# Kernel optimization log

Hardware: AMD Instinct MI355X
Metric: run time of the kernel (lower is better)

The kernel has to match this reference:

```python
import jax, jax.numpy as jnp
import numpy as np

N = 65536   # nodes
E = 524288  # edges (avg degree 8)
IN, H, Z = 256, 128, 32
LN_EPS = 1e-5


def setup_inputs() -> dict:
    key = jax.random.key(0)
    ks = jax.random.split(key, 6)
    x = jax.random.normal(ks[0], (N, IN), jnp.float32)
    edge_index = jax.random.randint(ks[1], (2, E), 0, N, jnp.int32)
    W1 = jax.random.normal(ks[2], (IN, H), jnp.float32) / np.sqrt(IN)
    W2 = jax.random.normal(ks[3], (H, H), jnp.float32) / np.sqrt(H)
    W3 = jax.random.normal(ks[4], (H, Z), jnp.float32) / np.sqrt(H)
    return dict(
        x=x, edge_index=edge_index,
        ln_w=jnp.ones((IN,), jnp.float32), ln_b=jnp.zeros((IN,), jnp.float32),
        W1=W1, b1=jnp.zeros((H,), jnp.float32),
        W2=W2, b2=jnp.zeros((H,), jnp.float32),
        W3=W3, b3=jnp.zeros((Z,), jnp.float32),
    )


def _layer_norm(x, w, b):
    mu = jnp.mean(x, axis=-1, keepdims=True)
    var = jnp.mean(jnp.square(x - mu), axis=-1, keepdims=True)
    return (x - mu) * jax.lax.rsqrt(var + LN_EPS) * w + b


def _gcn_conv(x, W, b, src, dst, n):
    # PyG GCNConv: transform, add self-loops, symmetric deg normalization, scatter-add.
    x = x @ W  # [N, out]
    ones = jnp.ones(src.shape[0], x.dtype)
    deg = jax.ops.segment_sum(ones, dst, num_segments=n) + 1.0  # +1 self-loop
    dis = jax.lax.rsqrt(deg)  # deg^{-1/2}
    norm = dis[src] * dis[dst]  # [E]
    agg = jax.ops.segment_sum(x[src] * norm[:, None], dst, num_segments=n)
    agg = agg + x * (dis * dis)[:, None]  # self-loop term: dis[i]*dis[i]
    return agg + b


def reference(x, edge_index, ln_w, ln_b, W1, b1, W2, b2, W3, b3):
    src, dst = edge_index[0], edge_index[1]
    n = x.shape[0]
    h = _layer_norm(x, ln_w, ln_b)
    h = jax.nn.relu(_gcn_conv(h, W1, b1, src, dst, n))
    # dropout is identity in eval mode
    h = jax.nn.relu(_gcn_conv(h, W2, b2, src, dst, n))
    return _gcn_conv(h, W3, b3, src, dst, n)
```

## Files before the change

### kernel.cpp

```cpp
#include <hip/hip_runtime.h>
#include <hip/hip_bf16.h>

#define FIN 256
#define FH 128
#define FZ 32

typedef unsigned short u16;
typedef unsigned int u32;
typedef __attribute__((ext_vector_type(4))) float f32x4;
typedef __attribute__((ext_vector_type(8))) _Float16 f16x8;
typedef __attribute__((ext_vector_type(4))) _Float16 f16x4;
typedef __attribute__((ext_vector_type(4))) unsigned int uint4v;

__device__ inline u16 f2h(float v) { return __builtin_bit_cast(u16, (_Float16)v); }

__global__ __launch_bounds__(256) void prep(const float* __restrict__ W1,
                                            const float* __restrict__ W2,
                                            const float* __restrict__ W3,
                                            u16* __restrict__ w1h, u16* __restrict__ w2h,
                                            u16* __restrict__ w3h, int* __restrict__ deg,
                                            int* __restrict__ total) {
    int b = blockIdx.x, t = threadIdx.x;
    if (b < 256) {
        deg[b * 256 + t] = 0;
        if (b == 0 && t == 0) *total = 0;
        return;
    }
    int i = (b - 256) * 256 + t;
    if (i < FIN * FH) {
        int k = i / FH, n = i % FH;
        w1h[n * FIN + k] = f2h(W1[i]);
    } else if (i < FIN * FH + FH * FH) {
        int j = i - FIN * FH;
        int k = j / FH, n = j % FH;
        w2h[n * FH + k] = f2h(W2[j]);
    } else {
        int j = i - (FIN * FH + FH * FH);
        int k = j / FZ, n = j % FZ;
        w3h[n * FH + k] = f2h(W3[j]);
    }
}

__global__ void deg_count(const int* __restrict__ dst, int* __restrict__ deg,
                          int* __restrict__ erank, int E) {
    int e = blockIdx.x * 256 + threadIdx.x;
    if (e < E) erank[e] = atomicAdd(&deg[dst[e]], 1);
}

__global__ __launch_bounds__(256) void scan_fused(const int* __restrict__ deg,
                                                  int* __restrict__ total,
                                                  int* __restrict__ rowstart,
                                                  float* __restrict__ dis) {
    __shared__ int s[256];
    __shared__ int base;
    int t = threadIdx.x;
    int i = blockIdx.x * 256 + t;
    int v = deg[i];
    s[t] = v;
    __syncthreads();
    for (int o = 1; o < 256; o <<= 1) {
        int add = (t >= o) ? s[t - o] : 0;
        __syncthreads();
        s[t] += add;
        __syncthreads();
    }
    if (t == 255) base = atomicAdd(total, s[255]);
    __syncthreads();
    rowstart[i] = s[t] - v + base;
    dis[i] = rsqrtf((float)v + 1.0f);
}

template <int K, int N, bool LN, bool FILL>
__global__ __launch_bounds__(512) void gemm_v5(
    const float* __restrict__ Xf, const u16* __restrict__ Xh, const u16* __restrict__ Wg,
    const float* __restrict__ lnw, const float* __restrict__ lnb,
    const float* __restrict__ dis, u16* __restrict__ Y,
    const int* __restrict__ src, const int* __restrict__ dst,
    const int* __restrict__ erank, const int* __restrict__ rowstart,
    int* __restrict__ csrc, int E) {
    constexpr int BM = 128;
    constexpr int NT = N / 16;

    extern __shared__ char smem[];
    u16* Wl = (u16*)smem;
    float* stats = (float*)(smem + (size_t)N * K * 2);
    float* lnwl = stats + (LN ? BM * 2 : 0);
    float* lnbl = lnwl + (LN ? K : 0);

    const int t = threadIdx.x;
    const int row0 = blockIdx.x * BM;

    if (FILL) {
        int epb = E / gridDim.x;
        int base = blockIdx.x * epb;
#pragma unroll
        for (int j = 0; j < 2; ++j) {
            int e = base + j * 512 + t;
            int d = dst[e];
            csrc[rowstart[d] + erank[e]] = src[e];
        }
    }

    for (int i = t; i < N * K / 8; i += 512) {
        int n = i / (K / 8), k8 = i % (K / 8);
        *(uint4v*)&Wl[n * K + ((k8 ^ (n & 7)) * 8)] = *(const uint4v*)&Wg[n * K + k8 * 8];
    }

    if (LN) {
        if (t < K / 4) {
            *(f32x4*)&lnwl[t * 4] = *(const f32x4*)&lnw[t * 4];
            *(f32x4*)&lnbl[t * 4] = *(const f32x4*)&lnb[t * 4];
        }
        int r = t >> 2, q = t & 3;
        const float* xr = Xf + (long long)(row0 + r) * K + q * (K / 4);
        float s = 0.f, ss = 0.f;
#pragma unroll
        for (int j = 0; j < K / 16; ++j) {
            f32x4 f = *(const f32x4*)(xr + j * 4);
#pragma unroll
            for (int c = 0; c < 4; ++c) {
                s += f[c];
                ss += f[c] * f[c];
            }
        }
        s += __shfl_xor(s, 1);
        ss += __shfl_xor(ss, 1);
        s += __shfl_xor(s, 2);
        ss += __shfl_xor(ss, 2);
        if (q == 0) {
            float mu = s * (1.0f / K);
            float var = ss * (1.0f / K) - mu * mu;
            stats[r * 2] = mu;
            stats[r * 2 + 1] = rsqrtf(fmaxf(var, 0.f) + 1e-5f);
        }
    }
    __syncthreads();

    const int wave = t >> 6, l = t & 63;
    const int lm = l & 15, lq = l >> 4;
    const int row = row0 + wave * 16 + lm;

    float mu = 0.f, rs = 1.f;
    if (LN) {
        mu = stats[(wave * 16 + lm) * 2];
        rs = stats[(wave * 16 + lm) * 2 + 1];
    }

    f32x4 acc[NT];
#pragma unroll
    for (int i = 0; i < NT; ++i) acc[i] = (f32x4){0.f, 0.f, 0.f, 0.f};

#pragma unroll
    for (int kk = 0; kk < K / 32; ++kk) {
        f16x8 a;
        if (LN) {
            const float* xr = Xf + (long long)row * K;
            f32x4 a0 = *(const f32x4*)(xr + kk * 32 + lq * 8);
            f32x4 a1 = *(const f32x4*)(xr + kk * 32 + lq * 8 + 4);
            f32x4 w0 = *(const f32x4*)&lnwl[kk * 32 + lq * 8];
            f32x4 w1 = *(const f32x4*)&lnwl[kk * 32 + lq * 8 + 4];
            f32x4 c0 = *(const f32x4*)&lnbl[kk * 32 + lq * 8];
            f32x4 c1 = *(const f32x4*)&lnbl[kk * 32 + lq * 8 + 4];
#pragma unroll
            for (int c = 0; c < 4; ++c) {
                a[c] = (_Float16)((a0[c] - mu) * rs * w0[c] + c0[c]);
                a[4 + c] = (_Float16)((a1[c] - mu) * rs * w1[c] + c1[c]);
            }
        } else {
            a = *(const f16x8*)&Xh[(long long)row * K + kk * 32 + lq * 8];
        }

#pragma unroll
        for (int nt = 0; nt < NT; ++nt) {
            int n = nt * 16 + lm;
            int off = n * K + (((kk * 4 + lq) ^ (n & 7)) * 8);
            f16x8 bh = *(const f16x8*)&Wl[off];
            acc[nt] = __builtin_amdgcn_mfma_f32_16x16x32_f16(a, bh, acc[nt], 0, 0, 0);
        }
    }

    const int mbase = row0 + wave * 16 + lq * 4;
    f32x4 d4 = *(const f32x4*)(dis + mbase);
#pragma unroll
    for (int nt = 0; nt < NT; ++nt) {
        int c = nt * 16 + lm;
#pragma unroll
        for (int r = 0; r < 4; ++r) Y[(long long)(mbase + r) * N + c] = f2h(acc[nt][r] * d4[r]);
    }
}

__global__ __launch_bounds__(256) void agg128h(
    const u16* __restrict__ T, const int* __restrict__ rowstart, const int* __restrict__ degv,
    const int* __restrict__ csrc, const float* __restrict__ dis, const float* __restrict__ bias,
    u16* __restrict__ OUT, int relu) {
    int node = blockIdx.x * 4 + (threadIdx.x >> 6);
    int l = threadIdx.x & 63;
    int h = l >> 4, c = l & 15;
    float di = dis[node];
    float acc[8] = {0.f, 0.f, 0.f, 0.f, 0.f, 0.f, 0.f, 0.f};
    if (h == 0) {
        f16x8 s = *(const f16x8*)&T[(long long)node * 128 + c * 8];
#pragma unroll
        for (int i = 0; i < 8; ++i) acc[i] = (float)s[i];
    }
    int e0 = rowstart[node];
    int e1 = e0 + degv[node];
    int e = e0 + h;
    for (; e + 4 < e1; e += 8) {
        int s0 = csrc[e], s1 = csrc[e + 4];
        f16x8 u0 = *(const f16x8*)&T[(long long)s0 * 128 + c * 8];
        f16x8 u1 = *(const f16x8*)&T[(long long)s1 * 128 + c * 8];
#pragma unroll
        for (int i = 0; i < 8; ++i) acc[i] += (float)u0[i] + (float)u1[i];
    }
    if (e < e1) {
        int s0 = csrc[e];
        f16x8 u0 = *(const f16x8*)&T[(long long)s0 * 128 + c * 8];
#pragma unroll
        for (int i = 0; i < 8; ++i) acc[i] += (float)u0[i];
    }
#pragma unroll
    for (int m = 16; m <= 32; m <<= 1) {
#pragma unroll
        for (int i = 0; i < 8; ++i) acc[i] += __shfl_xor(acc[i], m);
    }
    if (h == 0) {
        f32x4 b0 = *(const f32x4*)(bias + c * 8);
        f32x4 b1 = *(const f32x4*)(bias + c * 8 + 4);
        f16x8 r;
#pragma unroll
        for (int i = 0; i < 8; ++i) {
            float b = (i < 4) ? b0[i] : b1[i - 4];
            float v = acc[i] * di + b;
            if (relu) v = fmaxf(v, 0.f);
            r[i] = (_Float16)v;
        }
        *(f16x8*)&OUT[(long long)node * 128 + c * 8] = r;
    }
}

__global__ __launch_bounds__(256) void agg32h(
    const u16* __restrict__ T, const int* __restrict__ rowstart, const int* __restrict__ degv,
    const int* __restrict__ csrc, const float* __restrict__ dis, const float* __restrict__ bias,
    float* __restrict__ OUT) {
    int node = blockIdx.x * 4 + (threadIdx.x >> 6);
    int l = threadIdx.x & 63;
    int h = l >> 3, c = l & 7;
    float di = dis[node];
    f32x4 acc = (f32x4){0.f, 0.f, 0.f, 0.f};
    if (h == 0) {
        f16x4 s = *(const f16x4*)&T[(long long)node * 32 + c * 4];
#pragma unroll
        for (int i = 0; i < 4; ++i) acc[i] = (float)s[i];
    }
    int e0 = rowstart[node];
    int e1 = e0 + degv[node];
    int e = e0 + h;
    for (; e + 8 < e1; e += 16) {
        int s0 = csrc[e], s1 = csrc[e + 8];
        f16x4 u0 = *(const f16x4*)&T[(long long)s0 * 32 + c * 4];
        f16x4 u1 = *(const f16x4*)&T[(long long)s1 * 32 + c * 4];
#pragma unroll
        for (int i = 0; i < 4; ++i) acc[i] += (float)u0[i] + (float)u1[i];
    }
    if (e < e1) {
        int s0 = csrc[e];
        f16x4 u0 = *(const f16x4*)&T[(long long)s0 * 32 + c * 4];
#pragma unroll
        for (int i = 0; i < 4; ++i) acc[i] += (float)u0[i];
    }
#pragma unroll
    for (int m = 8; m <= 32; m <<= 1) {
#pragma unroll
        for (int i = 0; i < 4; ++i) acc[i] += __shfl_xor(acc[i], m);
    }
    if (h == 0) {
        f32x4 b0 = *(const f32x4*)(bias + c * 4);
        f32x4 r;
#pragma unroll
        for (int i = 0; i < 4; ++i) r[i] = acc[i] * di + b0[i];
        *(f32x4*)(OUT + (long long)node * 32 + c * 4) = r;
    }
}

extern "C" void kernel_launch(void* const* d_in, const int* in_sizes, int n_in,
                              void* d_out, int out_size, void* d_ws, size_t ws_size,
                              hipStream_t stream) {
    const float* x = (const float*)d_in[0];
    const int* ei = (const int*)d_in[1];
    const float* lnw = (const float*)d_in[2];
    const float* lnb = (const float*)d_in[3];
    const float* W1 = (const float*)d_in[4];
    const float* b1 = (const float*)d_in[5];
    const float* W2 = (const float*)d_in[6];
    const float* b2 = (const float*)d_in[7];
    const float* W3 = (const float*)d_in[8];
    const float* b3 = (const float*)d_in[9];
    float* out = (float*)d_out;

    const int n = in_sizes[0] / FIN;
    const int E = in_sizes[1] / 2;
    const int* src = ei;
    const int* dst = ei + E;

    char* w = (char*)d_ws;
    auto alloc = [&](size_t bytes) {
        char* p = w;
        w += (bytes + 255) & ~(size_t)255;
        return p;
    };
    int* deg = (int*)alloc((size_t)n * 4);
    int* rowstart = (int*)alloc((size_t)n * 4);
    int* erank = (int*)alloc((size_t)E * 4);
    int* total = (int*)alloc(256);
    float* dis = (float*)alloc((size_t)n * 4);
    int* csrc = (int*)alloc((size_t)E * 4);
    u16* w1h = (u16*)alloc(FIN * FH * 2);
    u16* w2h = (u16*)alloc(FH * FH * 2);
    u16* w3h = (u16*)alloc(FH * FZ * 2);
    u16* bufA = (u16*)alloc((size_t)n * FH * 2);
    u16* bufB = (u16*)alloc((size_t)n * FH * 2);

    const int lds1 = FIN * FH * 2 + 128 * 2 * 4 + 2 * FIN * 4;
    const int lds2 = FH * FH * 2;
    const int lds3 = FZ * FH * 2;
    hipFuncSetAttribute((const void*)&gemm_v5<256, 128, true, true>,
                        hipFuncAttributeMaxDynamicSharedMemorySize, lds1);
    hipFuncSetAttribute((const void*)&gemm_v5<128, 128, false, false>,
                        hipFuncAttributeMaxDynamicSharedMemorySize, lds2);
    hipFuncSetAttribute((const void*)&gemm_v5<128, 32, false, false>,
                        hipFuncAttributeMaxDynamicSharedMemorySize, lds3);

    prep<<<464, 256, 0, stream>>>(W1, W2, W3, w1h, w2h, w3h, deg, total);
    deg_count<<<E / 256, 256, 0, stream>>>(dst, deg, erank, E);
    scan_fused<<<n / 256, 256, 0, stream>>>(deg, total, rowstart, dis);
    gemm_v5<256, 128, true, true><<<n / 128, 512, lds1, stream>>>(
        x, nullptr, w1h, lnw, lnb, dis, bufA, src, dst, erank, rowstart, csrc, E);
    agg128h<<<n / 4, 256, 0, stream>>>(bufA, rowstart, deg, csrc, dis, b1, bufB, 1);
    gemm_v5<128, 128, false, false><<<n / 128, 512, lds2, stream>>>(
        nullptr, bufB, w2h, nullptr, nullptr, dis, bufA, nullptr, nullptr, nullptr, nullptr, nullptr, 0);
    agg128h<<<n / 4, 256, 0, stream>>>(bufA, rowstart, deg, csrc, dis, b2, bufB, 1);
    gemm_v5<128, 32, false, false><<<n / 128, 512, lds3, stream>>>(
        nullptr, bufB, w3h, nullptr, nullptr, dis, bufA, nullptr, nullptr, nullptr, nullptr, nullptr, 0);
    agg32h<<<n / 4, 256, 0, stream>>>(bufA, rowstart, deg, csrc, dis, b3, out);
}
```

Before: 176.3 us.

## Read GEMM weights directly from global in MFMA-chunked layout, drop LDS staging

Reorders the fp16 weight matrices in prep into K-chunks of 32 so each MFMA B fragment is one contiguous 16-byte global load, and removes the per-block copy of the weights into LDS. The MFMA operands are swapped (weights as A, activations as B), so each lane holds four consecutive output columns of one row and can write them as a single packed f16x4 store. LayerNorm weights and biases are also read straight from global memory. This removes the LDS fill and the barrier cost of every block and frees LDS for occupancy, but every wave now re-reads the weights through the L1/L2 caches.

```diff
diff --git a/kernel.cpp b/kernel.cpp
--- a/kernel.cpp
+++ b/kernel.cpp
@@ -10,15 +10,14 @@
 typedef __attribute__((ext_vector_type(4))) float f32x4;
 typedef __attribute__((ext_vector_type(8))) _Float16 f16x8;
 typedef __attribute__((ext_vector_type(4))) _Float16 f16x4;
-typedef __attribute__((ext_vector_type(4))) unsigned int uint4v;
 
 __device__ inline u16 f2h(float v) { return __builtin_bit_cast(u16, (_Float16)v); }
 
 __global__ __launch_bounds__(256) void prep(const float* __restrict__ W1,
                                             const float* __restrict__ W2,
                                             const float* __restrict__ W3,
-                                            u16* __restrict__ w1h, u16* __restrict__ w2h,
-                                            u16* __restrict__ w3h, int* __restrict__ deg,
+                                            u16* __restrict__ w1c, u16* __restrict__ w2c,
+                                            u16* __restrict__ w3c, int* __restrict__ deg,
                                             int* __restrict__ total) {
     int b = blockIdx.x, t = threadIdx.x;
     if (b < 256) {
@@ -29,15 +28,15 @@
     int i = (b - 256) * 256 + t;
     if (i < FIN * FH) {
         int k = i / FH, n = i % FH;
-        w1h[n * FIN + k] = f2h(W1[i]);
+        w1c[(k >> 5) * FH * 32 + n * 32 + (k & 31)] = f2h(W1[i]);
     } else if (i < FIN * FH + FH * FH) {
         int j = i - FIN * FH;
         int k = j / FH, n = j % FH;
-        w2h[n * FH + k] = f2h(W2[j]);
+        w2c[(k >> 5) * FH * 32 + n * 32 + (k & 31)] = f2h(W2[j]);
     } else {
         int j = i - (FIN * FH + FH * FH);
         int k = j / FZ, n = j % FZ;
-        w3h[n * FH + k] = f2h(W3[j]);
+        w3c[(k >> 5) * FZ * 32 + n * 32 + (k & 31)] = f2h(W3[j]);
     }
 }
 
@@ -71,8 +70,8 @@
 }
 
 template <int K, int N, bool LN, bool FILL>
-__global__ __launch_bounds__(512) void gemm_v5(
-    const float* __restrict__ Xf, const u16* __restrict__ Xh, const u16* __restrict__ Wg,
+__global__ __launch_bounds__(512) void gemm_v6(
+    const float* __restrict__ Xf, const u16* __restrict__ Xh, const u16* __restrict__ Wc,
     const float* __restrict__ lnw, const float* __restrict__ lnb,
     const float* __restrict__ dis, u16* __restrict__ Y,
     const int* __restrict__ src, const int* __restrict__ dst,
@@ -81,11 +80,7 @@
     constexpr int BM = 128;
     constexpr int NT = N / 16;
 
-    extern __shared__ char smem[];
-    u16* Wl = (u16*)smem;
-    float* stats = (float*)(smem + (size_t)N * K * 2);
-    float* lnwl = stats + (LN ? BM * 2 : 0);
-    float* lnbl = lnwl + (LN ? K : 0);
+    __shared__ float stats[BM * 2];
 
     const int t = threadIdx.x;
     const int row0 = blockIdx.x * BM;
@@ -101,16 +96,7 @@
         }
     }
 
-    for (int i = t; i < N * K / 8; i += 512) {
-        int n = i / (K / 8), k8 = i % (K / 8);
-        *(uint4v*)&Wl[n * K + ((k8 ^ (n & 7)) * 8)] = *(const uint4v*)&Wg[n * K + k8 * 8];
-    }
-
     if (LN) {
-        if (t < K / 4) {
-            *(f32x4*)&lnwl[t * 4] = *(const f32x4*)&lnw[t * 4];
-            *(f32x4*)&lnbl[t * 4] = *(const f32x4*)&lnb[t * 4];
-        }
         int r = t >> 2, q = t & 3;
         const float* xr = Xf + (long long)(row0 + r) * K + q * (K / 4);
         float s = 0.f, ss = 0.f;
@@ -133,8 +119,8 @@
             stats[r * 2] = mu;
             stats[r * 2 + 1] = rsqrtf(fmaxf(var, 0.f) + 1e-5f);
         }
-    }
-    __syncthreads();
+        __syncthreads();
+    }
 
     const int wave = t >> 6, l = t & 63;
     const int lm = l & 15, lq = l >> 4;
@@ -157,10 +143,10 @@
             const float* xr = Xf + (long long)row * K;
             f32x4 a0 = *(const f32x4*)(xr + kk * 32 + lq * 8);
             f32x4 a1 = *(const f32x4*)(xr + kk * 32 + lq * 8 + 4);
-            f32x4 w0 = *(const f32x4*)&lnwl[kk * 32 + lq * 8];
-            f32x4 w1 = *(const f32x4*)&lnwl[kk * 32 + lq * 8 + 4];
-            f32x4 c0 = *(const f32x4*)&lnbl[kk * 32 + lq * 8];
-            f32x4 c1 = *(const f32x4*)&lnbl[kk * 32 + lq * 8 + 4];
+            f32x4 w0 = *(const f32x4*)(lnw + kk * 32 + lq * 8);
+            f32x4 w1 = *(const f32x4*)(lnw + kk * 32 + lq * 8 + 4);
+            f32x4 c0 = *(const f32x4*)(lnb + kk * 32 + lq * 8);
+            f32x4 c1 = *(const f32x4*)(lnb + kk * 32 + lq * 8 + 4);
 #pragma unroll
             for (int c = 0; c < 4; ++c) {
                 a[c] = (_Float16)((a0[c] - mu) * rs * w0[c] + c0[c]);
@@ -172,20 +158,19 @@
 
 #pragma unroll
         for (int nt = 0; nt < NT; ++nt) {
-            int n = nt * 16 + lm;
-            int off = n * K + (((kk * 4 + lq) ^ (n & 7)) * 8);
-            f16x8 bh = *(const f16x8*)&Wl[off];
-            acc[nt] = __builtin_amdgcn_mfma_f32_16x16x32_f16(a, bh, acc[nt], 0, 0, 0);
-        }
-    }
-
-    const int mbase = row0 + wave * 16 + lq * 4;
-    f32x4 d4 = *(const f32x4*)(dis + mbase);
+            f16x8 wv = *(const f16x8*)&Wc[((kk * N) + nt * 16 + lm) * 32 + lq * 8];
+            acc[nt] = __builtin_amdgcn_mfma_f32_16x16x32_f16(wv, a, acc[nt], 0, 0, 0);
+        }
+    }
+
+    const float di = dis[row];
+    u16* yr = Y + (long long)row * N;
 #pragma unroll
     for (int nt = 0; nt < NT; ++nt) {
-        int c = nt * 16 + lm;
-#pragma unroll
-        for (int r = 0; r < 4; ++r) Y[(long long)(mbase + r) * N + c] = f2h(acc[nt][r] * d4[r]);
+        f16x4 v;
+#pragma unroll
+        for (int r = 0; r < 4; ++r) v[r] = (_Float16)(acc[nt][r] * di);
+        *(f16x4*)&yr[nt * 16 + lq * 4] = v;
     }
 }
 
@@ -315,32 +300,22 @@
     int* total = (int*)alloc(256);
     float* dis = (float*)alloc((size_t)n * 4);
     int* csrc = (int*)alloc((size_t)E * 4);
-    u16* w1h = (u16*)alloc(FIN * FH * 2);
-    u16* w2h = (u16*)alloc(FH * FH * 2);
-    u16* w3h = (u16*)alloc(FH * FZ * 2);
+    u16* w1c = (u16*)alloc(FIN * FH * 2);
+    u16* w2c = (u16*)alloc(FH * FH * 2);
+    u16* w3c = (u16*)alloc(FH * FZ * 2);
     u16* bufA = (u16*)alloc((size_t)n * FH * 2);
     u16* bufB = (u16*)alloc((size_t)n * FH * 2);
 
-    const int lds1 = FIN * FH * 2 + 128 * 2 * 4 + 2 * FIN * 4;
-    const int lds2 = FH * FH * 2;
-    const int lds3 = FZ * FH * 2;
-    hipFuncSetAttribute((const void*)&gemm_v5<256, 128, true, true>,
-                        hipFuncAttributeMaxDynamicSharedMemorySize, lds1);
-    hipFuncSetAttribute((const void*)&gemm_v5<128, 128, false, false>,
-                        hipFuncAttributeMaxDynamicSharedMemorySize, lds2);
-    hipFuncSetAttribute((const void*)&gemm_v5<128, 32, false, false>,
-                        hipFuncAttributeMaxDynamicSharedMemorySize, lds3);
-
-    prep<<<464, 256, 0, stream>>>(W1, W2, W3, w1h, w2h, w3h, deg, total);
+    prep<<<464, 256, 0, stream>>>(W1, W2, W3, w1c, w2c, w3c, deg, total);
     deg_count<<<E / 256, 256, 0, stream>>>(dst, deg, erank, E);
     scan_fused<<<n / 256, 256, 0, stream>>>(deg, total, rowstart, dis);
-    gemm_v5<256, 128, true, true><<<n / 128, 512, lds1, stream>>>(
-        x, nullptr, w1h, lnw, lnb, dis, bufA, src, dst, erank, rowstart, csrc, E);
+    gemm_v6<256, 128, true, true><<<n / 128, 512, 0, stream>>>(
+        x, nullptr, w1c, lnw, lnb, dis, bufA, src, dst, erank, rowstart, csrc, E);
     agg128h<<<n / 4, 256, 0, stream>>>(bufA, rowstart, deg, csrc, dis, b1, bufB, 1);
-    gemm_v5<128, 128, false, false><<<n / 128, 512, lds2, stream>>>(
-        nullptr, bufB, w2h, nullptr, nullptr, dis, bufA, nullptr, nullptr, nullptr, nullptr, nullptr, 0);
+    gemm_v6<128, 128, false, false><<<n / 128, 512, 0, stream>>>(
+        nullptr, bufB, w2c, nullptr, nullptr, dis, bufA, nullptr, nullptr, nullptr, nullptr, nullptr, 0);
     agg128h<<<n / 4, 256, 0, stream>>>(bufA, rowstart, deg, csrc, dis, b2, bufB, 1);
-    gemm_v5<128, 32, false, false><<<n / 128, 512, lds3, stream>>>(
-        nullptr, bufB, w3h, nullptr, nullptr, dis, bufA, nullptr, nullptr, nullptr, nullptr, nullptr, 0);
+    gemm_v6<128, 32, false, false><<<n / 128, 512, 0, stream>>>(
+        nullptr, bufB, w3c, nullptr, nullptr, dis, bufA, nullptr, nullptr, nullptr, nullptr, nullptr, 0);
     agg32h<<<n / 4, 256, 0, stream>>>(bufA, rowstart, deg, csrc, dis, b3, out);
 }
```

New measurement: 199.1 us. +12.9%, slower.
